# Optimization experiments

Hardware: AMD Instinct MI355X
Metric: run time of the kernel (lower is better)

The kernel has to match this reference:

```python
import jax, jax.numpy as jnp
import numpy as np

N = 100000   # nodes
E = 1600000  # edges
G = 256      # graphs in batch
C_IN = 128
D = 64
EPS = 1e-5
SLOPE = 0.01  # torch LeakyReLU default


def gcn_conv(h_x, src, dst, w_edge, W, b):
    """GCNConv: linear -> symmetric-normalized scatter aggregation (+ self loops) -> bias."""
    n = h_x.shape[0]
    h = h_x @ W                                   # [N, D]
    # add self loops with weight 1
    loop = jnp.arange(n, dtype=src.dtype)
    s = jnp.concatenate([src, loop])
    d = jnp.concatenate([dst, loop])
    w = jnp.concatenate([w_edge, jnp.ones((n,), h_x.dtype)])
    deg = jax.ops.segment_sum(w, d, num_segments=n)  # degree on target nodes
    dinv = jnp.where(deg > 0, jax.lax.rsqrt(jnp.maximum(deg, 1e-12)), 0.0)
    norm = dinv[s] * w * dinv[d]                  # [E+N]
    msg = h[s] * norm[:, None]                    # gather + scale
    out = jax.ops.segment_sum(msg, d, num_segments=n)
    return out + b


def batch_norm(h, gamma, beta):
    mean = jnp.mean(h, axis=0)
    var = jnp.mean((h - mean) ** 2, axis=0)       # biased var (training-mode BN)
    return (h - mean) * jax.lax.rsqrt(var + EPS) * gamma + beta


def setup_inputs() -> dict:
    key = jax.random.key(0)
    ks = jax.random.split(key, 16)
    inp = {
        "x": jax.random.normal(ks[0], (N, C_IN), jnp.float32),
        "edge_index": jax.random.randint(ks[1], (2, E), 0, N, jnp.int32),
        "batch": jnp.sort(jax.random.randint(ks[2], (N,), 0, G, jnp.int32)),
        "edge_attr": jax.random.uniform(ks[3], (E,), jnp.float32),
        "W0": jax.random.normal(ks[4], (C_IN, D), jnp.float32) * 0.05,
        "b0": jnp.zeros((D,), jnp.float32),
        "g0": jnp.ones((D,), jnp.float32),
        "be0": jnp.zeros((D,), jnp.float32),
        "W1": jax.random.normal(ks[5], (D, D), jnp.float32) * 0.05,
        "b1": jnp.zeros((D,), jnp.float32),
        "g1": jnp.ones((D,), jnp.float32),
        "be1": jnp.zeros((D,), jnp.float32),
        "W2": jax.random.normal(ks[6], (D, D), jnp.float32) * 0.05,
        "b2": jnp.zeros((D,), jnp.float32),
        "W3": jax.random.normal(ks[7], (D, D), jnp.float32) * 0.05,
        "b3": jnp.zeros((D,), jnp.float32),
        "Wfc": jax.random.normal(ks[8], (2 * D, 1), jnp.float32) * 0.05,
        "bfc": jnp.zeros((1,), jnp.float32),
    }
    return inp


def reference(x, edge_index, batch, edge_attr,
              W0, b0, g0, be0, W1, b1, g1, be1, W2, b2, W3, b3, Wfc, bfc):
    src, dst = edge_index[0], edge_index[1]
    lrelu = lambda h: jax.nn.leaky_relu(h, SLOPE)

    h = lrelu(batch_norm(gcn_conv(x, src, dst, edge_attr, W0, b0), g0, be0))
    h = lrelu(batch_norm(gcn_conv(h, src, dst, edge_attr, W1, b1), g1, be1))
    h = lrelu(gcn_conv(h, src, dst, edge_attr, W2, b2))  # dropout is identity in eval
    h = lrelu(gcn_conv(h, src, dst, edge_attr, W3, b3))

    mx = jax.ops.segment_max(h, batch, num_segments=G)
    sm = jax.ops.segment_sum(h, batch, num_segments=G)
    cnt = jax.ops.segment_sum(jnp.ones((N,), h.dtype), batch, num_segments=G)
    mean = sm / jnp.maximum(cnt, 1.0)[:, None]
    pooled = jnp.concatenate([mx, mean], axis=1)   # [G, 2D]
    return pooled @ Wfc + bfc                      # [G, 1]
```

## Files before the change

kernel.cpp:

```cpp
#include <hip/hip_runtime.h>
#include <math.h>

#define LRELU_SLOPE 0.01f
#define BN_EPS 1e-5f
#define WQ_SCALE 1048576.0f
#define WQ_INV   9.5367431640625e-7f

static inline int ceil_div(int a, int b) { return (a + b - 1) / b; }

typedef _Float16 f16;
typedef f16 h4_t __attribute__((ext_vector_type(4)));
typedef f16 h8_t __attribute__((ext_vector_type(8)));
typedef float f32x4 __attribute__((ext_vector_type(4)));

__device__ __forceinline__ unsigned short f2bf(float f) {
  unsigned int u = __float_as_uint(f);
  u = u + 0x7FFFu + ((u >> 16) & 1u);
  return (unsigned short)(u >> 16);
}
#define BF2F(u) __uint_as_float(((unsigned int)(u)) << 16)

__launch_bounds__(1024)
__global__ void b1_hist(const int* __restrict__ ei, int* __restrict__ histT,
                        int E, int chunk, int nbuck) {
  __shared__ unsigned int hist[1024];
  const int t = threadIdx.x;
  const int blk = blockIdx.x;
  hist[t] = 0;
  __syncthreads();
  const int e0 = blk * chunk;
  const int e1 = min(e0 + chunk, E);
  for (int e = e0 + t; e < e1; e += 1024) {
    int d = ei[E + e];
    atomicAdd(&hist[d >> 7], 1u);
  }
  __syncthreads();
  if (t < nbuck) histT[(size_t)t * 256 + blk] = (int)hist[t];
}

__global__ void scan1i(const int* __restrict__ in, int* __restrict__ out,
                       int* __restrict__ bsum, int n) {
  __shared__ int lds[256];
  const int t = threadIdx.x;
  const int base = blockIdx.x * 1024 + t * 4;
  int v0 = 0, v1 = 0, v2 = 0, v3 = 0;
  if (base + 0 < n) v0 = in[base + 0];
  if (base + 1 < n) v1 = in[base + 1];
  if (base + 2 < n) v2 = in[base + 2];
  if (base + 3 < n) v3 = in[base + 3];
  int s = v0 + v1 + v2 + v3;
  lds[t] = s;
  __syncthreads();
#pragma unroll
  for (int off = 1; off < 256; off <<= 1) {
    int y = 0;
    if (t >= off) y = lds[t - off];
    __syncthreads();
    if (t >= off) lds[t] += y;
    __syncthreads();
  }
  int incl = lds[t];
  int excl = incl - s;
  if (base + 0 < n) out[base + 0] = excl;
  if (base + 1 < n) out[base + 1] = excl + v0;
  if (base + 2 < n) out[base + 2] = excl + v0 + v1;
  if (base + 3 < n) out[base + 3] = excl + v0 + v1 + v2;
  if (t == 255) bsum[blockIdx.x] = incl;
}

__global__ void scan2i(int* __restrict__ bsum, int nb) {
  __shared__ int lds[256];
  int t = threadIdx.x;
  int v = (t < nb) ? bsum[t] : 0;
  lds[t] = v;
  __syncthreads();
#pragma unroll
  for (int off = 1; off < 256; off <<= 1) {
    int y = 0;
    if (t >= off) y = lds[t - off];
    __syncthreads();
    if (t >= off) lds[t] += y;
    __syncthreads();
  }
  if (t < nb) bsum[t] = lds[t] - v;
}

__global__ void scan3i(int* __restrict__ data, const int* __restrict__ bscan, int n) {
  int i = blockIdx.x * blockDim.x + threadIdx.x;
  if (i < n) data[i] += bscan[i >> 10];
}

__launch_bounds__(1024)
__global__ void b3_scatter(const int* __restrict__ ei, const float* __restrict__ w,
                           const int* __restrict__ histS,
                           unsigned long long* __restrict__ bucketed,
                           int E, int chunk, int nbuck) {
  __shared__ unsigned int cursor[1024];
  const int t = threadIdx.x;
  const int blk = blockIdx.x;
  cursor[t] = (t < nbuck) ? (unsigned int)histS[(size_t)t * 256 + blk] : 0u;
  __syncthreads();
  const int e0 = blk * chunk;
  const int e1 = min(e0 + chunk, E);
  for (int e = e0 + t; e < e1; e += 1024) {
    int s = ei[e];
    int d = ei[E + e];
    unsigned int pos = atomicAdd(&cursor[d >> 7], 1u);
    unsigned long long p = ((unsigned long long)(unsigned int)(d & 127) << 57) |
                           ((unsigned long long)(unsigned int)s << 32) |
                           (unsigned long long)__float_as_uint(w[e]);
    bucketed[pos] = p;
  }
}

__launch_bounds__(256)
__global__ void c1_degree(const unsigned long long* __restrict__ bucketed,
                          const int* __restrict__ histS,
                          int* __restrict__ rowstart, float* __restrict__ dinv,
                          int N, int E, int nbuck) {
  __shared__ unsigned int cnt[128], wsum[128];
  __shared__ int sc[128];
  const int t = threadIdx.x;
  const int b = blockIdx.x;
  if (t < 128) { cnt[t] = 0; wsum[t] = 0; }
  __syncthreads();
  const int r0 = histS[(size_t)b * 256];
  const int r1 = (b + 1 < nbuck) ? histS[(size_t)(b + 1) * 256] : E;
  for (int r = r0 + t; r < r1; r += 256) {
    unsigned long long p = bucketed[r];
    int d7 = (int)(p >> 57);
    float wv = __uint_as_float((unsigned int)p);
    atomicAdd(&cnt[d7], 1u);
    atomicAdd(&wsum[d7], (unsigned int)__float2uint_rn(wv * WQ_SCALE));
  }
  __syncthreads();
  if (t < 128) sc[t] = (int)cnt[t];
  __syncthreads();
#pragma unroll
  for (int off = 1; off < 128; off <<= 1) {
    int y = 0;
    if (t < 128 && t >= off) y = sc[t - off];
    __syncthreads();
    if (t < 128 && t >= off) sc[t] += y;
    __syncthreads();
  }
  if (t < 128) {
    int node = (b << 7) + t;
    if (node < N) {
      rowstart[node] = r0 + sc[t] - (int)cnt[t];
      float deg = 1.0f + (float)wsum[t] * WQ_INV;
      dinv[node] = rsqrtf(deg);
    }
  }
  if (b == 0 && t == 0) rowstart[N] = E;
}

__launch_bounds__(256)
__global__ void c2_fill(const unsigned long long* __restrict__ bucketed,
                        const int* __restrict__ histS,
                        const int* __restrict__ rowstart, const float* __restrict__ dinv,
                        unsigned long long* __restrict__ colval,
                        int N, int E, int nbuck) {
  __shared__ unsigned int cursor[128];
  const int t = threadIdx.x;
  const int b = blockIdx.x;
  if (t < 128) {
    int node = (b << 7) + t;
    cursor[t] = (node < N) ? (unsigned int)rowstart[node] : 0u;
  }
  __syncthreads();
  const int r0 = histS[(size_t)b * 256];
  const int r1 = (b + 1 < nbuck) ? histS[(size_t)(b + 1) * 256] : E;
  for (int r = r0 + t; r < r1; r += 256) {
    unsigned long long p = bucketed[r];
    int d7 = (int)(p >> 57);
    int s = (int)((p >> 32) & 0x1FFFFFF);
    float wv = __uint_as_float((unsigned int)p);
    unsigned int pos = atomicAdd(&cursor[d7], 1u);
    float v = wv * dinv[s];
    colval[pos] = ((unsigned long long)(unsigned int)s << 32) |
                  (unsigned long long)__float_as_uint(v);
  }
}

template <int K, int BN>
__launch_bounds__(256, 4)
__global__ void k_gemm(const float* __restrict__ X, const float* __restrict__ W,
                       unsigned short* __restrict__ H16,
                       const float* __restrict__ s, const float* __restrict__ ss,
                       const float* __restrict__ g, const float* __restrict__ be,
                       int N) {
  constexpr int KP = K + 8;
  constexpr int KQ = K / 4;
  __shared__ f16 Xl[64 * KP];
  __shared__ f16 Wt[64 * KP];
  __shared__ float scaleC[64], shiftC[64];
  const int t = threadIdx.x;
  const int n0 = blockIdx.x * 64;

  if (BN) {
    if (t < 64) {
      float invN = 1.0f / (float)N;
      float mean = s[t] * invN;
      float var = ss[t] * invN - mean * mean;
      float sc = g[t] * rsqrtf(var + BN_EPS);
      scaleC[t] = sc;
      shiftC[t] = be[t] - mean * sc;
    }
    __syncthreads();
  }

  for (int idx = t; idx < 64 * KQ; idx += 256) {
    int row = idx / KQ;
    int kq = idx % KQ;
    int gn = n0 + row;
    float4 v = make_float4(0.f, 0.f, 0.f, 0.f);
    if (gn < N) v = *(const float4*)(X + (size_t)gn * K + 4 * kq);
    if (BN) {
      int c = 4 * kq;
      float a;
      a = v.x * scaleC[c + 0] + shiftC[c + 0]; v.x = (a > 0.f) ? a : LRELU_SLOPE * a;
      a = v.y * scaleC[c + 1] + shiftC[c + 1]; v.y = (a > 0.f) ? a : LRELU_SLOPE * a;
      a = v.z * scaleC[c + 2] + shiftC[c + 2]; v.z = (a > 0.f) ? a : LRELU_SLOPE * a;
      a = v.w * scaleC[c + 3] + shiftC[c + 3]; v.w = (a > 0.f) ? a : LRELU_SLOPE * a;
    }
    h4_t hv = { (f16)v.x, (f16)v.y, (f16)v.z, (f16)v.w };
    *(h4_t*)(Xl + row * KP + 4 * kq) = hv;
  }
  for (int idx = t; idx < K * 16; idx += 256) {
    int k = idx >> 4;
    int c4 = idx & 15;
    float4 wv = *(const float4*)(W + (size_t)k * 64 + 4 * c4);
    Wt[(4 * c4 + 0) * KP + k] = (f16)wv.x;
    Wt[(4 * c4 + 1) * KP + k] = (f16)wv.y;
    Wt[(4 * c4 + 2) * KP + k] = (f16)wv.z;
    Wt[(4 * c4 + 3) * KP + k] = (f16)wv.w;
  }
  __syncthreads();

  const int lane = t & 63;
  const int wv = t >> 6;
  const int fr = lane & 15;
  const int fc = lane >> 4;

  f32x4 acc0 = {0.f, 0.f, 0.f, 0.f};
  f32x4 acc1 = {0.f, 0.f, 0.f, 0.f};
  f32x4 acc2 = {0.f, 0.f, 0.f, 0.f};
  f32x4 acc3 = {0.f, 0.f, 0.f, 0.f};

  const f16* ap = Xl + (16 * wv + fr) * KP + 8 * fc;
  const f16* bp0 = Wt + (0 + fr) * KP + 8 * fc;
  const f16* bp1 = Wt + (16 + fr) * KP + 8 * fc;
  const f16* bp2 = Wt + (32 + fr) * KP + 8 * fc;
  const f16* bp3 = Wt + (48 + fr) * KP + 8 * fc;

#pragma unroll
  for (int kt = 0; kt < K; kt += 32) {
    h8_t a = *(const h8_t*)(ap + kt);
    acc0 = __builtin_amdgcn_mfma_f32_16x16x32_f16(a, *(const h8_t*)(bp0 + kt), acc0, 0, 0, 0);
    acc1 = __builtin_amdgcn_mfma_f32_16x16x32_f16(a, *(const h8_t*)(bp1 + kt), acc1, 0, 0, 0);
    acc2 = __builtin_amdgcn_mfma_f32_16x16x32_f16(a, *(const h8_t*)(bp2 + kt), acc2, 0, 0, 0);
    acc3 = __builtin_amdgcn_mfma_f32_16x16x32_f16(a, *(const h8_t*)(bp3 + kt), acc3, 0, 0, 0);
  }

#pragma unroll
  for (int r = 0; r < 4; ++r) {
    int node = n0 + 16 * wv + 4 * fc + r;
    if (node < N) {
      size_t base = (size_t)node * 64 + fr;
      H16[base + 0]  = f2bf(acc0[r]);
      H16[base + 16] = f2bf(acc1[r]);
      H16[base + 32] = f2bf(acc2[r]);
      H16[base + 48] = f2bf(acc3[r]);
    }
  }
}

#define AGG_GATH2(cv) (*(const unsigned int*)(hcol + ((size_t)((cv) >> 32)) * 64))
#define AGG_FMA2(a, cv, u)                                        \
  {                                                               \
    float v_ = __uint_as_float((unsigned int)(cv));               \
    (a).x += v_ * __uint_as_float((u) << 16);                     \
    (a).y += v_ * __uint_as_float((u) & 0xffff0000u);             \
  }
template <int STATS, int LRELU>
__launch_bounds__(256, 4)
__global__ void k_agg(const unsigned short* __restrict__ h16, float* __restrict__ hout,
                      const float* __restrict__ bias, const float* __restrict__ dinv,
                      const int* __restrict__ rowstart,
                      const unsigned long long* __restrict__ colval,
                      float* __restrict__ partial, int N) {
  __shared__ float2 rs[STATS ? 256 : 1];
  __shared__ float2 rq[STATS ? 256 : 1];
  const int t = threadIdx.x;
  const int grp = t >> 5;
  const int lane = t & 31;
  const int d = blockIdx.x * 8 + grp;
  const bool valid = (d < N);
  int r0 = 0, r1 = 0;
  if (valid) { r0 = rowstart[d]; r1 = rowstart[d + 1]; }
  const unsigned short* hcol = h16 + lane * 2;
  float2 a0 = make_float2(0.f, 0.f);
  float2 a1 = make_float2(0.f, 0.f);
  float2 a2 = make_float2(0.f, 0.f);
  float2 a3 = make_float2(0.f, 0.f);
  int r = r0;
  for (; r + 8 <= r1; r += 8) {
    unsigned long long cv0 = colval[r + 0];
    unsigned long long cv1 = colval[r + 1];
    unsigned long long cv2 = colval[r + 2];
    unsigned long long cv3 = colval[r + 3];
    unsigned long long cv4 = colval[r + 4];
    unsigned long long cv5 = colval[r + 5];
    unsigned long long cv6 = colval[r + 6];
    unsigned long long cv7 = colval[r + 7];
    unsigned int u0 = AGG_GATH2(cv0);
    unsigned int u1 = AGG_GATH2(cv1);
    unsigned int u2 = AGG_GATH2(cv2);
    unsigned int u3 = AGG_GATH2(cv3);
    unsigned int u4 = AGG_GATH2(cv4);
    unsigned int u5 = AGG_GATH2(cv5);
    unsigned int u6 = AGG_GATH2(cv6);
    unsigned int u7 = AGG_GATH2(cv7);
    AGG_FMA2(a0, cv0, u0); AGG_FMA2(a1, cv1, u1);
    AGG_FMA2(a2, cv2, u2); AGG_FMA2(a3, cv3, u3);
    AGG_FMA2(a0, cv4, u4); AGG_FMA2(a1, cv5, u5);
    AGG_FMA2(a2, cv6, u6); AGG_FMA2(a3, cv7, u7);
  }
  for (; r + 4 <= r1; r += 4) {
    unsigned long long cv0 = colval[r + 0];
    unsigned long long cv1 = colval[r + 1];
    unsigned long long cv2 = colval[r + 2];
    unsigned long long cv3 = colval[r + 3];
    unsigned int u0 = AGG_GATH2(cv0);
    unsigned int u1 = AGG_GATH2(cv1);
    unsigned int u2 = AGG_GATH2(cv2);
    unsigned int u3 = AGG_GATH2(cv3);
    AGG_FMA2(a0, cv0, u0); AGG_FMA2(a1, cv1, u1);
    AGG_FMA2(a2, cv2, u2); AGG_FMA2(a3, cv3, u3);
  }
  for (; r < r1; ++r) {
    unsigned long long cv = colval[r];
    unsigned int u = AGG_GATH2(cv);
    AGG_FMA2(a0, cv, u);
  }
  float2 acc;
  acc.x = (a0.x + a1.x) + (a2.x + a3.x);
  acc.y = (a0.y + a1.y) + (a2.y + a3.y);
  float di = valid ? dinv[d] : 0.f;
  float di2 = di * di;
  unsigned int hd = 0u;
  if (valid) hd = *(const unsigned int*)(hcol + (size_t)d * 64);
  float2 b2 = *(const float2*)(bias + lane * 2);
  float2 o;
  o.x = di * acc.x + di2 * __uint_as_float(hd << 16) + b2.x;
  o.y = di * acc.y + di2 * __uint_as_float(hd & 0xffff0000u) + b2.y;
  if (LRELU) {
    o.x = (o.x > 0.f) ? o.x : LRELU_SLOPE * o.x;
    o.y = (o.y > 0.f) ? o.y : LRELU_SLOPE * o.y;
  }
  if (!valid) o = make_float2(0.f, 0.f);
  if (valid) *(float2*)(hout + (size_t)d * 64 + lane * 2) = o;

  if (STATS) {
    rs[t] = o;
    rq[t] = make_float2(o.x * o.x, o.y * o.y);
    __syncthreads();
#pragma unroll
    for (int st = 4; st >= 1; st >>= 1) {
      if (grp < st) {
        float2 sa = rs[t], sb = rs[t + st * 32];
        float2 qa = rq[t], qb = rq[t + st * 32];
        rs[t] = make_float2(sa.x + sb.x, sa.y + sb.y);
        rq[t] = make_float2(qa.x + qb.x, qa.y + qb.y);
      }
      __syncthreads();
    }
    if (t < 32) {
      float2 sv = rs[t], qv = rq[t];
      float* ps = partial + (size_t)blockIdx.x * 128;
      ps[2 * t + 0] = sv.x;
      ps[2 * t + 1] = sv.y;
      ps[64 + 2 * t + 0] = qv.x;
      ps[64 + 2 * t + 1] = qv.y;
    }
  }
}

__global__ void k_stats_reduce(const float* __restrict__ partial, float* __restrict__ s,
                               float* __restrict__ ss, int nb) {
  __shared__ float red[256];
  const int c = blockIdx.x;
  const int t = threadIdx.x;
  float a = 0.f;
  for (int b = t; b < nb; b += 256) a += partial[(size_t)b * 128 + c];
  red[t] = a;
  __syncthreads();
  for (int st = 128; st >= 1; st >>= 1) {
    if (t < st) red[t] += red[t + st];
    __syncthreads();
  }
  if (t == 0) {
    if (c < 64) s[c] = red[0];
    else ss[c - 64] = red[0];
  }
}

__global__ void k_gbounds(const int* __restrict__ batch, int* __restrict__ gstart,
                          int N, int G) {
  int i = blockIdx.x * blockDim.x + threadIdx.x;
  if (i >= N) return;
  int b = batch[i];
  int prev = (i == 0) ? -1 : batch[i - 1];
  for (int g = prev + 1; g <= b; ++g) gstart[g] = i;
  if (i == N - 1) {
    for (int g = b + 1; g <= G; ++g) gstart[g] = N;
  }
}

__launch_bounds__(256)
__global__ void k_pool(const float* __restrict__ h, const int* __restrict__ gstart,
                       const float* __restrict__ Wfc, const float* __restrict__ bfc,
                       float* __restrict__ out, int G) {
  __shared__ float lmx[256], lsm[256], red[128];
  const int g = blockIdx.x;
  const int t = threadIdx.x;
  const int c = t & 63;
  const int sub = t >> 6;
  const int n0 = gstart[g];
  const int n1 = gstart[g + 1];
  float mx = -INFINITY, sm = 0.f;
  for (int n = n0 + sub; n < n1; n += 4) {
    float v = h[(size_t)n * 64 + c];
    mx = fmaxf(mx, v);
    sm += v;
  }
  lmx[t] = mx;
  lsm[t] = sm;
  __syncthreads();
  if (t < 64) {
    mx = fmaxf(fmaxf(lmx[t], lmx[t + 64]), fmaxf(lmx[t + 128], lmx[t + 192]));
    sm = lsm[t] + lsm[t + 64] + lsm[t + 128] + lsm[t + 192];
    float cntf = (float)(n1 - n0);
    float mean = sm / fmaxf(cntf, 1.0f);
    red[t] = mx * Wfc[t];
    red[t + 64] = mean * Wfc[64 + t];
  }
  __syncthreads();
  for (int st = 64; st >= 1; st >>= 1) {
    if (t < st) red[t] += red[t + st];
    __syncthreads();
  }
  if (t == 0) out[g] = red[0] + bfc[0];
}

extern "C" void kernel_launch(void* const* d_in, const int* in_sizes, int n_in,
                              void* d_out, int out_size, void* d_ws, size_t ws_size,
                              hipStream_t stream) {
  const float* x = (const float*)d_in[0];
  const int* ei = (const int*)d_in[1];
  const int* batch = (const int*)d_in[2];
  const float* eattr = (const float*)d_in[3];
  const float* W0 = (const float*)d_in[4];
  const float* b0 = (const float*)d_in[5];
  const float* g0 = (const float*)d_in[6];
  const float* be0 = (const float*)d_in[7];
  const float* W1 = (const float*)d_in[8];
  const float* b1 = (const float*)d_in[9];
  const float* g1 = (const float*)d_in[10];
  const float* be1 = (const float*)d_in[11];
  const float* W2 = (const float*)d_in[12];
  const float* b2 = (const float*)d_in[13];
  const float* W3 = (const float*)d_in[14];
  const float* b3 = (const float*)d_in[15];
  const float* Wfc = (const float*)d_in[16];
  const float* bfc = (const float*)d_in[17];
  float* out = (float*)d_out;

  const int N = in_sizes[2];
  const int E = in_sizes[3];
  const int CIN = in_sizes[0] / N;
  const int G = out_size;
  const int nbuck = ceil_div(N, 128);
  const int chunk = ceil_div(E, 256);
  const int M = nbuck * 256;
  const int nag = ceil_div(N, 8);

  size_t off = 0;
  auto alloc = [&](size_t bytes) -> void* {
    void* p = (char*)d_ws + off;
    off += (bytes + 255) & ~(size_t)255;
    return p;
  };
  int* histT = (int*)alloc((size_t)1024 * 256 * 4);
  int* histS = (int*)alloc((size_t)1024 * 256 * 4);
  int* bsum = (int*)alloc(1024 * 4);
  unsigned long long* bucketed = (unsigned long long*)alloc((size_t)E * 8);
  float* dinv = (float*)alloc((size_t)N * 4);
  int* rowstart = (int*)alloc((size_t)(N + 1) * 4);
  unsigned long long* colval = (unsigned long long*)alloc((size_t)E * 8);
  float* A = (float*)alloc((size_t)N * 64 * 4);
  float* B = (float*)alloc((size_t)N * 64 * 4);
  unsigned short* H16 = (unsigned short*)alloc((size_t)N * 64 * 2);
  float* sums = (float*)alloc(256 * 4);
  float* partial = (float*)alloc((size_t)nag * 128 * 4);
  int* gstart = (int*)alloc((size_t)(G + 1) * 4);
  (void)ws_size; (void)n_in; (void)CIN;

  b1_hist<<<256, 1024, 0, stream>>>(ei, histT, E, chunk, nbuck);
  const int nbs = ceil_div(M, 1024);
  scan1i<<<nbs, 256, 0, stream>>>(histT, histS, bsum, M);
  scan2i<<<1, 256, 0, stream>>>(bsum, nbs);
  scan3i<<<ceil_div(M, 256), 256, 0, stream>>>(histS, bsum, M);
  b3_scatter<<<256, 1024, 0, stream>>>(ei, eattr, histS, bucketed, E, chunk, nbuck);
  c1_degree<<<nbuck, 256, 0, stream>>>(bucketed, histS, rowstart, dinv, N, E, nbuck);
  c2_fill<<<nbuck, 256, 0, stream>>>(bucketed, histS, rowstart, dinv, colval, N, E, nbuck);
  k_gbounds<<<ceil_div(N, 256), 256, 0, stream>>>(batch, gstart, N, G);

  k_gemm<128, 0><<<ceil_div(N, 64), 256, 0, stream>>>(x, W0, H16, nullptr, nullptr, nullptr, nullptr, N);
  k_agg<1, 0><<<nag, 256, 0, stream>>>(H16, B, b0, dinv, rowstart, colval, partial, N);
  k_stats_reduce<<<128, 256, 0, stream>>>(partial, sums + 0, sums + 64, nag);

  k_gemm<64, 1><<<ceil_div(N, 64), 256, 0, stream>>>(B, W1, H16, sums + 0, sums + 64, g0, be0, N);
  k_agg<1, 0><<<nag, 256, 0, stream>>>(H16, A, b1, dinv, rowstart, colval, partial, N);
  k_stats_reduce<<<128, 256, 0, stream>>>(partial, sums + 128, sums + 192, nag);

  k_gemm<64, 1><<<ceil_div(N, 64), 256, 0, stream>>>(A, W2, H16, sums + 128, sums + 192, g1, be1, N);
  k_agg<0, 1><<<nag, 256, 0, stream>>>(H16, B, b2, dinv, rowstart, colval, nullptr, N);

  k_gemm<64, 0><<<ceil_div(N, 64), 256, 0, stream>>>(B, W3, H16, nullptr, nullptr, nullptr, nullptr, N);
  k_agg<0, 1><<<nag, 256, 0, stream>>>(H16, A, b3, dinv, rowstart, colval, nullptr, N);

  k_pool<<<G, 256, 0, stream>>>(A, gstart, Wfc, bfc, out, G);
}
```

Measured before the change: 470.1 us.

## Stage neighbor rows into LDS via global_load_lds in persistent wave-per-node aggregation

Rewrites the CSR aggregation kernel so each 64-lane wave handles one destination node in a grid-stride loop over a fixed 2048-block grid. Up to 32 neighbor bf16 rows are fetched per batch with global_load_lds, so each 128-byte row lands directly in shared memory, then accumulated one feature per lane. BN statistics are accumulated per thread across nodes and reduced once per block. The goal is to cut register-held gathers and raise memory-level parallelism, but each batch waits for all loads (vmcnt(0)) before computing, and the inner loop needs a shuffle per edge.

Measured after the change: 502.0 us. 1.07x slower.

```diff
diff --git a/kernel.cpp b/kernel.cpp
--- a/kernel.cpp
+++ b/kernel.cpp
@@ -12,6 +12,9 @@
 typedef f16 h4_t __attribute__((ext_vector_type(4)));
 typedef f16 h8_t __attribute__((ext_vector_type(8)));
 typedef float f32x4 __attribute__((ext_vector_type(4)));
+
+typedef const __attribute__((address_space(1))) void* as1cp;
+typedef __attribute__((address_space(3))) void* as3p;
 
 __device__ __forceinline__ unsigned short f2bf(float f) {
   unsigned int u = __float_as_uint(f);
@@ -276,113 +279,69 @@
   }
 }
 
-#define AGG_GATH2(cv) (*(const unsigned int*)(hcol + ((size_t)((cv) >> 32)) * 64))
-#define AGG_FMA2(a, cv, u)                                        \
-  {                                                               \
-    float v_ = __uint_as_float((unsigned int)(cv));               \
-    (a).x += v_ * __uint_as_float((u) << 16);                     \
-    (a).y += v_ * __uint_as_float((u) & 0xffff0000u);             \
-  }
 template <int STATS, int LRELU>
-__launch_bounds__(256, 4)
+__launch_bounds__(256)
 __global__ void k_agg(const unsigned short* __restrict__ h16, float* __restrict__ hout,
                       const float* __restrict__ bias, const float* __restrict__ dinv,
                       const int* __restrict__ rowstart,
                       const unsigned long long* __restrict__ colval,
                       float* __restrict__ partial, int N) {
-  __shared__ float2 rs[STATS ? 256 : 1];
-  __shared__ float2 rq[STATS ? 256 : 1];
-  const int t = threadIdx.x;
-  const int grp = t >> 5;
-  const int lane = t & 31;
-  const int d = blockIdx.x * 8 + grp;
-  const bool valid = (d < N);
-  int r0 = 0, r1 = 0;
-  if (valid) { r0 = rowstart[d]; r1 = rowstart[d + 1]; }
-  const unsigned short* hcol = h16 + lane * 2;
-  float2 a0 = make_float2(0.f, 0.f);
-  float2 a1 = make_float2(0.f, 0.f);
-  float2 a2 = make_float2(0.f, 0.f);
-  float2 a3 = make_float2(0.f, 0.f);
-  int r = r0;
-  for (; r + 8 <= r1; r += 8) {
-    unsigned long long cv0 = colval[r + 0];
-    unsigned long long cv1 = colval[r + 1];
-    unsigned long long cv2 = colval[r + 2];
-    unsigned long long cv3 = colval[r + 3];
-    unsigned long long cv4 = colval[r + 4];
-    unsigned long long cv5 = colval[r + 5];
-    unsigned long long cv6 = colval[r + 6];
-    unsigned long long cv7 = colval[r + 7];
-    unsigned int u0 = AGG_GATH2(cv0);
-    unsigned int u1 = AGG_GATH2(cv1);
-    unsigned int u2 = AGG_GATH2(cv2);
-    unsigned int u3 = AGG_GATH2(cv3);
-    unsigned int u4 = AGG_GATH2(cv4);
-    unsigned int u5 = AGG_GATH2(cv5);
-    unsigned int u6 = AGG_GATH2(cv6);
-    unsigned int u7 = AGG_GATH2(cv7);
-    AGG_FMA2(a0, cv0, u0); AGG_FMA2(a1, cv1, u1);
-    AGG_FMA2(a2, cv2, u2); AGG_FMA2(a3, cv3, u3);
-    AGG_FMA2(a0, cv4, u4); AGG_FMA2(a1, cv5, u5);
-    AGG_FMA2(a2, cv6, u6); AGG_FMA2(a3, cv7, u7);
-  }
-  for (; r + 4 <= r1; r += 4) {
-    unsigned long long cv0 = colval[r + 0];
-    unsigned long long cv1 = colval[r + 1];
-    unsigned long long cv2 = colval[r + 2];
-    unsigned long long cv3 = colval[r + 3];
-    unsigned int u0 = AGG_GATH2(cv0);
-    unsigned int u1 = AGG_GATH2(cv1);
-    unsigned int u2 = AGG_GATH2(cv2);
-    unsigned int u3 = AGG_GATH2(cv3);
-    AGG_FMA2(a0, cv0, u0); AGG_FMA2(a1, cv1, u1);
-    AGG_FMA2(a2, cv2, u2); AGG_FMA2(a3, cv3, u3);
-  }
-  for (; r < r1; ++r) {
-    unsigned long long cv = colval[r];
-    unsigned int u = AGG_GATH2(cv);
-    AGG_FMA2(a0, cv, u);
-  }
-  float2 acc;
-  acc.x = (a0.x + a1.x) + (a2.x + a3.x);
-  acc.y = (a0.y + a1.y) + (a2.y + a3.y);
-  float di = valid ? dinv[d] : 0.f;
-  float di2 = di * di;
-  unsigned int hd = 0u;
-  if (valid) hd = *(const unsigned int*)(hcol + (size_t)d * 64);
-  float2 b2 = *(const float2*)(bias + lane * 2);
-  float2 o;
-  o.x = di * acc.x + di2 * __uint_as_float(hd << 16) + b2.x;
-  o.y = di * acc.y + di2 * __uint_as_float(hd & 0xffff0000u) + b2.y;
-  if (LRELU) {
-    o.x = (o.x > 0.f) ? o.x : LRELU_SLOPE * o.x;
-    o.y = (o.y > 0.f) ? o.y : LRELU_SLOPE * o.y;
-  }
-  if (!valid) o = make_float2(0.f, 0.f);
-  if (valid) *(float2*)(hout + (size_t)d * 64 + lane * 2) = o;
+  __shared__ unsigned short stage[4][2048];
+  __shared__ float sbuf[STATS ? 4 : 1][STATS ? 64 : 1];
+  __shared__ float qbuf[STATS ? 4 : 1][STATS ? 64 : 1];
+  const int t = threadIdx.x;
+  const int w = t >> 6;
+  const int lane = t & 63;
+  unsigned short* slds = &stage[w][0];
+  const float bv = bias[lane];
+  float sacc = 0.f, qacc = 0.f;
+  const int dstep = gridDim.x * 4;
+
+  for (int d = blockIdx.x * 4 + w; d < N; d += dstep) {
+    const int r0 = rowstart[d];
+    const int r1 = rowstart[d + 1];
+    float a = 0.f;
+    for (int rb = r0; rb < r1; rb += 32) {
+      const int bdeg = min(32, r1 - rb);
+      unsigned long long cv = 0ull;
+      if (lane < 32) cv = colval[rb + min(lane, bdeg - 1)];
+      unsigned int srcv = (unsigned int)(cv >> 32);
+      float wgt = __uint_as_float((unsigned int)cv);
+      const int npair = (bdeg + 1) >> 1;
+      const int halfoff = (lane >> 5) ? 1 : 0;
+      for (int j = 0; j < npair; ++j) {
+        unsigned int sA = __shfl(srcv, 2 * j);
+        unsigned int sB = __shfl(srcv, min(2 * j + 1, bdeg - 1));
+        unsigned int srow = halfoff ? sB : sA;
+        const char* gp = (const char*)h16 + (size_t)srow * 128 + (size_t)(lane & 31) * 4;
+        __builtin_amdgcn_global_load_lds((as1cp)gp, (as3p)(slds + j * 128), 4, 0, 0);
+      }
+      asm volatile("s_waitcnt vmcnt(0)" ::: "memory");
+      __builtin_amdgcn_sched_barrier(0);
+      for (int e = 0; e < bdeg; ++e) {
+        float ve = __shfl(wgt, e);
+        unsigned short u = slds[e * 64 + lane];
+        a += ve * BF2F(u);
+      }
+    }
+    const float di = dinv[d];
+    const float di2 = di * di;
+    unsigned short hd = h16[(size_t)d * 64 + lane];
+    float o = di * a + di2 * BF2F(hd) + bv;
+    if (LRELU) o = (o > 0.f) ? o : LRELU_SLOPE * o;
+    hout[(size_t)d * 64 + lane] = o;
+    if (STATS) { sacc += o; qacc += o * o; }
+  }
 
   if (STATS) {
-    rs[t] = o;
-    rq[t] = make_float2(o.x * o.x, o.y * o.y);
-    __syncthreads();
-#pragma unroll
-    for (int st = 4; st >= 1; st >>= 1) {
-      if (grp < st) {
-        float2 sa = rs[t], sb = rs[t + st * 32];
-        float2 qa = rq[t], qb = rq[t + st * 32];
-        rs[t] = make_float2(sa.x + sb.x, sa.y + sb.y);
-        rq[t] = make_float2(qa.x + qb.x, qa.y + qb.y);
-      }
-      __syncthreads();
-    }
-    if (t < 32) {
-      float2 sv = rs[t], qv = rq[t];
-      float* ps = partial + (size_t)blockIdx.x * 128;
-      ps[2 * t + 0] = sv.x;
-      ps[2 * t + 1] = sv.y;
-      ps[64 + 2 * t + 0] = qv.x;
-      ps[64 + 2 * t + 1] = qv.y;
+    sbuf[w][lane] = sacc;
+    qbuf[w][lane] = qacc;
+    __syncthreads();
+    if (t < 64) {
+      float sv = sbuf[0][t] + sbuf[1][t] + sbuf[2][t] + sbuf[3][t];
+      float qv = qbuf[0][t] + qbuf[1][t] + qbuf[2][t] + qbuf[3][t];
+      partial[(size_t)blockIdx.x * 128 + t] = sv;
+      partial[(size_t)blockIdx.x * 128 + 64 + t] = qv;
     }
   }
 }
@@ -484,7 +443,7 @@
   const int nbuck = ceil_div(N, 128);
   const int chunk = ceil_div(E, 256);
   const int M = nbuck * 256;
-  const int nag = ceil_div(N, 8);
+  const int nag = 2048;
 
   size_t off = 0;
   auto alloc = [&](size_t bytes) -> void* {
```
